# Kernel tuning notes

Hardware: AMD Instinct MI355X
Metric: run time of the kernel (lower is better)

Reference implementation:

```python
import jax, jax.numpy as jnp
import numpy as np

B, T, S, D = 8, 16, 256, 1024
H, KVH, HD = 16, 4, 64
GROUPS = H // KVH
SCALE = HD ** -0.5
CAP = 50.0
EPS = 1e-6


def setup_inputs() -> dict:
    key = jax.random.key(0)
    ks = jax.random.split(key, 5)
    return {
        "x": jax.random.normal(ks[0], (B, T, S, D), dtype=jnp.float32),
        "Wq": jax.random.normal(ks[1], (D, H * HD), dtype=jnp.float32) * (D ** -0.5),
        "Wk": jax.random.normal(ks[2], (D, KVH * HD), dtype=jnp.float32) * (D ** -0.5),
        "Wv": jax.random.normal(ks[3], (D, KVH * HD), dtype=jnp.float32) * (D ** -0.5),
        "Wo": jax.random.normal(ks[4], (H * HD, D), dtype=jnp.float32) * ((H * HD) ** -0.5),
        "q_norm_w": jnp.ones((HD,), dtype=jnp.float32),
        "k_norm_w": jnp.ones((HD,), dtype=jnp.float32),
    }


def _rmsnorm(x, w):
    rms = jnp.sqrt(jnp.mean(x * x, axis=-1, keepdims=True) + EPS)
    return x / rms * w


def reference(x, Wq, Wk, Wv, Wo, q_norm_w, k_norm_w):
    b, t, s, d = x.shape
    xf = x.reshape(b * t, s, d)                    # (BT, S, D)
    q = (xf @ Wq).reshape(b * t, s, H, HD).transpose(0, 2, 1, 3)   # (BT, H, S, hd)
    k = (xf @ Wk).reshape(b * t, s, KVH, HD).transpose(0, 2, 1, 3)  # (BT, KVH, S, hd)
    v = (xf @ Wv).reshape(b * t, s, KVH, HD).transpose(0, 2, 1, 3)
    q = _rmsnorm(q, q_norm_w)
    k = _rmsnorm(k, k_norm_w)
    if GROUPS > 1:
        k = jnp.repeat(k, GROUPS, axis=1)          # (BT, H, S, hd)
        v = jnp.repeat(v, GROUPS, axis=1)
    logits = jnp.einsum("bhqd,bhkd->bhqk", q, k) * SCALE
    logits = CAP * jnp.tanh(logits / CAP)          # soft cap
    attn = jax.nn.softmax(logits, axis=-1)
    out = jnp.einsum("bhqk,bhkd->bhqd", attn, v)   # (BT, H, S, hd)
    out = out.transpose(0, 2, 1, 3).reshape(b * t, s, H * HD)
    out = out @ Wo
    return out.reshape(b, t, s, d)
```

## Files before the change

### kernel.cpp

```cpp
#include <hip/hip_runtime.h>
#include <cstdint>
#include <cstddef>

typedef __bf16 bf16x8 __attribute__((ext_vector_type(8)));
typedef float f32x4 __attribute__((ext_vector_type(4)));
typedef unsigned short u16;
typedef unsigned short u16x8 __attribute__((ext_vector_type(8)));

#define ROWS 32768
#define DMODEL 1024
#define NQKV 1536
#define SCALE_ 0.125f
#define CAP_ 50.0f

__device__ __forceinline__ u16 f2bf(float f) {
    unsigned u = __float_as_uint(f);
    u += 0x7fffu + ((u >> 16) & 1u);
    return (u16)(u >> 16);
}
__device__ __forceinline__ float bf2f(u16 b) {
    return __uint_as_float(((unsigned)b) << 16);
}

__global__ __launch_bounds__(256) void f32_to_bf16_vec(
    const float* __restrict__ in, u16* __restrict__ out, int n4)
{
    int i = blockIdx.x * 256 + threadIdx.x;
    if (i >= n4) return;
    float4 f = ((const float4*)in)[i];
    ushort4 u;
    u.x = f2bf(f.x); u.y = f2bf(f.y); u.z = f2bf(f.z); u.w = f2bf(f.w);
    ((ushort4*)out)[i] = u;
}

__global__ __launch_bounds__(256) void transpose_bf16(
    const float* __restrict__ src, u16* __restrict__ dst, int R, int C)
{
    __shared__ float tile[32][33];
    int c0 = blockIdx.x * 32;
    int r0 = blockIdx.y * 32;
    int tx = threadIdx.x & 31;
    int ty = threadIdx.x >> 5;
#pragma unroll
    for (int i = 0; i < 32; i += 8)
        tile[ty + i][tx] = src[(size_t)(r0 + ty + i) * C + (c0 + tx)];
    __syncthreads();
#pragma unroll
    for (int i = 0; i < 32; i += 8)
        dst[(size_t)(c0 + ty + i) * R + (r0 + tx)] = f2bf(tile[tx][ty + i]);
}

template<bool BF16OUT>
__global__ __launch_bounds__(256) void gemm_bt(
    const u16* __restrict__ A, const u16* __restrict__ Bt,
    void* __restrict__ Cout, int M, int N, int K)
{
    __shared__ u16 As[128][32];
    __shared__ u16 Bs[128][32];
    const int tid  = threadIdx.x;
    const int wave = tid >> 6;
    const int lane = tid & 63;
    const int q4   = lane >> 4;
    const int cl   = lane & 15;
    const int wr   = wave >> 1, wc = wave & 1;
    const int m0   = blockIdx.x * 128;
    const int n0   = blockIdx.y * 128;
    const int srow = lane >> 2;
    const int skoff = (lane & 3) * 8;

    const f32x4 zero = {0.f, 0.f, 0.f, 0.f};
    f32x4 acc[4][4];
#pragma unroll
    for (int i = 0; i < 4; ++i)
#pragma unroll
        for (int j = 0; j < 4; ++j) acc[i][j] = zero;

    for (int k0 = 0; k0 < K; k0 += 32) {
        __syncthreads();
#pragma unroll
        for (int cc = 0; cc < 2; ++cc) {
            int r = 32 * wave + 16 * cc + srow;
            const u16* ga = A + (size_t)(m0 + r) * K + k0 + skoff;
            __builtin_amdgcn_global_load_lds(
                (const __attribute__((address_space(1))) void*)ga,
                (__attribute__((address_space(3))) void*)(&As[32 * wave + 16 * cc][0]),
                16, 0, 0);
            const u16* gb = Bt + (size_t)(n0 + r) * K + k0 + skoff;
            __builtin_amdgcn_global_load_lds(
                (const __attribute__((address_space(1))) void*)gb,
                (__attribute__((address_space(3))) void*)(&Bs[32 * wave + 16 * cc][0]),
                16, 0, 0);
        }
        __syncthreads();
        bf16x8 af[4], bfr[4];
#pragma unroll
        for (int i = 0; i < 4; ++i)
            af[i] = *(const bf16x8*)&As[64 * wr + 16 * i + cl][q4 * 8];
#pragma unroll
        for (int j = 0; j < 4; ++j)
            bfr[j] = *(const bf16x8*)&Bs[64 * wc + 16 * j + cl][q4 * 8];
#pragma unroll
        for (int i = 0; i < 4; ++i)
#pragma unroll
            for (int j = 0; j < 4; ++j)
                acc[i][j] = __builtin_amdgcn_mfma_f32_16x16x32_bf16(
                    af[i], bfr[j], acc[i][j], 0, 0, 0);
    }

#pragma unroll
    for (int i = 0; i < 4; ++i)
#pragma unroll
        for (int j = 0; j < 4; ++j)
#pragma unroll
            for (int r = 0; r < 4; ++r) {
                int row = m0 + 64 * wr + 16 * i + q4 * 4 + r;
                int col = n0 + 64 * wc + 16 * j + cl;
                if (BF16OUT)
                    ((u16*)Cout)[(size_t)row * N + col] = f2bf(acc[i][j][r]);
                else
                    ((float*)Cout)[(size_t)row * N + col] = acc[i][j][r];
            }
}

__global__ __launch_bounds__(256) void rmsnorm_qk(
    u16* __restrict__ qkv, const float* __restrict__ qw, const float* __restrict__ kw)
{
    int gid = blockIdx.x * 16 + (threadIdx.x >> 4);
    int l16 = threadIdx.x & 15;
    int row = gid / 20;
    int hc  = gid - row * 20;
    const float* w = (hc < 16) ? qw : kw;
    size_t base = (size_t)row * NQKV + hc * 64;
    u16* p = qkv + base + l16 * 4;
    uint2 d = *(const uint2*)p;
    float f0 = bf2f((u16)(d.x & 0xffff));
    float f1 = bf2f((u16)(d.x >> 16));
    float f2 = bf2f((u16)(d.y & 0xffff));
    float f3 = bf2f((u16)(d.y >> 16));
    float ss = f0 * f0 + f1 * f1 + f2 * f2 + f3 * f3;
#pragma unroll
    for (int off = 1; off < 16; off <<= 1) ss += __shfl_xor(ss, off, 64);
    float r = rsqrtf(ss * (1.0f / 64.0f) + 1e-6f);
    float w0 = w[l16 * 4 + 0], w1 = w[l16 * 4 + 1];
    float w2 = w[l16 * 4 + 2], w3 = w[l16 * 4 + 3];
    uint2 o;
    o.x = (unsigned)f2bf(f0 * r * w0) | ((unsigned)f2bf(f1 * r * w1) << 16);
    o.y = (unsigned)f2bf(f2 * r * w2) | ((unsigned)f2bf(f3 * r * w3) << 16);
    *(uint2*)p = o;
}

__global__ __launch_bounds__(256, 2) void attention_kernel(
    const u16* __restrict__ qkv, u16* __restrict__ ao)
{
    const int bi  = blockIdx.x;
    const int bt  = bi >> 4;
    const int h   = bi & 15;
    const int kvh = h >> 2;
    const int tid  = threadIdx.x;
    const int wave = tid >> 6;
    const int lane = tid & 63;
    const int q4   = lane >> 4;
    const int cl   = lane & 15;

    __shared__ u16 Vt[64][264];
    __shared__ u16 P[4][64][72];

    {
        const u16* vrow = qkv + (size_t)(bt * 256 + tid) * NQKV + 1280 + kvh * 64;
#pragma unroll
        for (int ch = 0; ch < 8; ++ch) {
            u16x8 v8 = *(const u16x8*)(vrow + ch * 8);
#pragma unroll
            for (int e = 0; e < 8; ++e) Vt[ch * 8 + e][tid] = v8[e];
        }
    }
    __syncthreads();

    const u16* qbase = qkv + (size_t)(bt * 256) * NQKV + h * 64;
    const u16* kbase = qkv + (size_t)(bt * 256) * NQKV + 1024 + kvh * 64;

    const f32x4 zero = {0.f, 0.f, 0.f, 0.f};
    f32x4 o[4][4];
    float m_[4][4], l_[4][4];
#pragma unroll
    for (int i = 0; i < 4; ++i)
#pragma unroll
        for (int r = 0; r < 4; ++r) { m_[i][r] = -1e30f; l_[i][r] = 0.f; }
#pragma unroll
    for (int i = 0; i < 4; ++i)
#pragma unroll
        for (int j = 0; j < 4; ++j) o[i][j] = zero;

    for (int nb = 0; nb < 4; ++nb) {
        f32x4 s[4][4];
#pragma unroll
        for (int i = 0; i < 4; ++i)
#pragma unroll
            for (int j = 0; j < 4; ++j) s[i][j] = zero;

#pragma unroll
        for (int ks = 0; ks < 2; ++ks) {
            bf16x8 qa[4], kb[4];
#pragma unroll
            for (int i = 0; i < 4; ++i)
                qa[i] = *(const bf16x8*)(qbase +
                    (size_t)(wave * 64 + 16 * i + cl) * NQKV + ks * 32 + q4 * 8);
#pragma unroll
            for (int j = 0; j < 4; ++j)
                kb[j] = *(const bf16x8*)(kbase +
                    (size_t)(nb * 64 + 16 * j + cl) * NQKV + ks * 32 + q4 * 8);
#pragma unroll
            for (int i = 0; i < 4; ++i)
#pragma unroll
                for (int j = 0; j < 4; ++j)
                    s[i][j] = __builtin_amdgcn_mfma_f32_16x16x32_bf16(
                        qa[i], kb[j], s[i][j], 0, 0, 0);
        }

        float bm[4][4];
#pragma unroll
        for (int i = 0; i < 4; ++i)
#pragma unroll
            for (int r = 0; r < 4; ++r) bm[i][r] = -1e30f;
#pragma unroll
        for (int i = 0; i < 4; ++i)
#pragma unroll
            for (int j = 0; j < 4; ++j)
#pragma unroll
                for (int r = 0; r < 4; ++r) {
                    float y = s[i][j][r] * (SCALE_ / CAP_);
                    float e = __expf(2.0f * y);
                    float capped = CAP_ * (1.0f - 2.0f / (e + 1.0f));
                    s[i][j][r] = capped;
                    bm[i][r] = fmaxf(bm[i][r], capped);
                }
#pragma unroll
        for (int off = 1; off < 16; off <<= 1)
#pragma unroll
            for (int i = 0; i < 4; ++i)
#pragma unroll
                for (int r = 0; r < 4; ++r)
                    bm[i][r] = fmaxf(bm[i][r], __shfl_xor(bm[i][r], off, 64));

        float alpha[4][4];
#pragma unroll
        for (int i = 0; i < 4; ++i)
#pragma unroll
            for (int r = 0; r < 4; ++r) {
                float mn = fmaxf(m_[i][r], bm[i][r]);
                alpha[i][r] = __expf(m_[i][r] - mn);
                m_[i][r] = mn;
            }
#pragma unroll
        for (int i = 0; i < 4; ++i)
#pragma unroll
            for (int j = 0; j < 4; ++j)
#pragma unroll
                for (int r = 0; r < 4; ++r) o[i][j][r] *= alpha[i][r];

        float rs[4][4];
#pragma unroll
        for (int i = 0; i < 4; ++i)
#pragma unroll
            for (int r = 0; r < 4; ++r) rs[i][r] = 0.f;
#pragma unroll
        for (int i = 0; i < 4; ++i)
#pragma unroll
            for (int j = 0; j < 4; ++j)
#pragma unroll
                for (int r = 0; r < 4; ++r) {
                    float p = __expf(s[i][j][r] - m_[i][r]);
                    s[i][j][r] = p;
                    rs[i][r] += p;
                }
#pragma unroll
        for (int off = 1; off < 16; off <<= 1)
#pragma unroll
            for (int i = 0; i < 4; ++i)
#pragma unroll
                for (int r = 0; r < 4; ++r) rs[i][r] += __shfl_xor(rs[i][r], off, 64);
#pragma unroll
        for (int i = 0; i < 4; ++i)
#pragma unroll
            for (int r = 0; r < 4; ++r) l_[i][r] = l_[i][r] * alpha[i][r] + rs[i][r];

#pragma unroll
        for (int i = 0; i < 4; ++i)
#pragma unroll
            for (int j = 0; j < 4; ++j)
#pragma unroll
                for (int r = 0; r < 4; ++r)
                    P[wave][16 * i + q4 * 4 + r][16 * j + cl] = f2bf(s[i][j][r]);
        __syncthreads();

#pragma unroll
        for (int ks = 0; ks < 2; ++ks) {
            bf16x8 pa[4], vb[4];
#pragma unroll
            for (int i = 0; i < 4; ++i)
                pa[i] = *(const bf16x8*)&P[wave][16 * i + cl][ks * 32 + q4 * 8];
#pragma unroll
            for (int j = 0; j < 4; ++j)
                vb[j] = *(const bf16x8*)&Vt[16 * j + cl][nb * 64 + ks * 32 + q4 * 8];
#pragma unroll
            for (int i = 0; i < 4; ++i)
#pragma unroll
                for (int j = 0; j < 4; ++j)
                    o[i][j] = __builtin_amdgcn_mfma_f32_16x16x32_bf16(
                        pa[i], vb[j], o[i][j], 0, 0, 0);
        }
    }

#pragma unroll
    for (int i = 0; i < 4; ++i)
#pragma unroll
        for (int r = 0; r < 4; ++r) {
            float inv = 1.0f / l_[i][r];
            int row = bt * 256 + wave * 64 + 16 * i + q4 * 4 + r;
#pragma unroll
            for (int j = 0; j < 4; ++j) {
                int col = h * 64 + 16 * j + cl;
                ao[(size_t)row * DMODEL + col] = f2bf(o[i][j][r] * inv);
            }
        }
}

extern "C" void kernel_launch(void* const* d_in, const int* in_sizes, int n_in,
                              void* d_out, int out_size, void* d_ws, size_t ws_size,
                              hipStream_t stream)
{
    const float* x  = (const float*)d_in[0];
    const float* Wq = (const float*)d_in[1];
    const float* Wk = (const float*)d_in[2];
    const float* Wv = (const float*)d_in[3];
    const float* Wo = (const float*)d_in[4];
    const float* qw = (const float*)d_in[5];
    const float* kw = (const float*)d_in[6];
    float* out = (float*)d_out;

    char* ws = (char*)d_ws;
    u16* Xb  = (u16*)(ws);
    u16* QKV = (u16*)(ws + (size_t)67108864);
    u16* AO  = (u16*)(ws + (size_t)167772160);
    u16* WcT = (u16*)(ws + (size_t)234881024);
    u16* WoT = (u16*)(ws + (size_t)238026752);

    f32_to_bf16_vec<<<dim3(32768), dim3(256), 0, stream>>>(x, Xb, 8388608);
    transpose_bf16<<<dim3(32, 32), dim3(256), 0, stream>>>(Wq, WcT, 1024, 1024);
    transpose_bf16<<<dim3(8, 32), dim3(256), 0, stream>>>(Wk, WcT + (size_t)1024 * 1024, 1024, 256);
    transpose_bf16<<<dim3(8, 32), dim3(256), 0, stream>>>(Wv, WcT + (size_t)1280 * 1024, 1024, 256);
    transpose_bf16<<<dim3(32, 32), dim3(256), 0, stream>>>(Wo, WoT, 1024, 1024);
    gemm_bt<true><<<dim3(256, 12), dim3(256), 0, stream>>>(Xb, WcT, (void*)QKV, ROWS, NQKV, 1024);
    rmsnorm_qk<<<dim3(40960), dim3(256), 0, stream>>>(QKV, qw, kw);
    attention_kernel<<<dim3(2048), dim3(256), 0, stream>>>(QKV, AO);
    gemm_bt<false><<<dim3(256, 8), dim3(256), 0, stream>>>(AO, WoT, (void*)out, ROWS, DMODEL, 1024);
}
```

Measured before the change: 683.3 us.

## Fuse QK RMSNorm into attention and use a fixed-max softcap softmax

Removes the separate rmsnorm_qk pass. Per-row Q and K RMS scales are now computed inside the attention kernel and applied to the logits, with the norm weights folded into Q. Because tanh soft-capping bounds the logits, online max tracking and rescaling are replaced by exponentiating the capped logit directly with exp2/rcp intrinsics. Row sums are computed with an MFMA against a ones vector instead of shuffles. The P tile shrinks, the block-wide barrier is dropped, and occupancy is raised to 3 blocks per SIMD; the risks are exp values up to e^50 being held in bf16 and extra register pressure.

```diff
diff --git a/kernel.cpp b/kernel.cpp
--- a/kernel.cpp
+++ b/kernel.cpp
@@ -5,21 +5,25 @@
 typedef __bf16 bf16x8 __attribute__((ext_vector_type(8)));
 typedef float f32x4 __attribute__((ext_vector_type(4)));
 typedef unsigned short u16;
+typedef unsigned int u32;
 typedef unsigned short u16x8 __attribute__((ext_vector_type(8)));
 
 #define ROWS 32768
 #define DMODEL 1024
 #define NQKV 1536
-#define SCALE_ 0.125f
-#define CAP_ 50.0f
+#define C1_ 0.0072134752044448170f
+#define A2_ 144.26950408889634f
+#define B2_ 72.13475204444817f
 
 __device__ __forceinline__ u16 f2bf(float f) {
     unsigned u = __float_as_uint(f);
     u += 0x7fffu + ((u >> 16) & 1u);
     return (u16)(u >> 16);
 }
-__device__ __forceinline__ float bf2f(u16 b) {
-    return __uint_as_float(((unsigned)b) << 16);
+__device__ __forceinline__ float bf_lo(u32 u) { return __uint_as_float(u << 16); }
+__device__ __forceinline__ float bf_hi(u32 u) { return __uint_as_float(u & 0xffff0000u); }
+__device__ __forceinline__ u32 pack_rne(float lo, float hi) {
+    return (u32)f2bf(lo) | ((u32)f2bf(hi) << 16);
 }
 
 __global__ __launch_bounds__(256) void f32_to_bf16_vec(
@@ -122,35 +126,9 @@
             }
 }
 
-__global__ __launch_bounds__(256) void rmsnorm_qk(
-    u16* __restrict__ qkv, const float* __restrict__ qw, const float* __restrict__ kw)
-{
-    int gid = blockIdx.x * 16 + (threadIdx.x >> 4);
-    int l16 = threadIdx.x & 15;
-    int row = gid / 20;
-    int hc  = gid - row * 20;
-    const float* w = (hc < 16) ? qw : kw;
-    size_t base = (size_t)row * NQKV + hc * 64;
-    u16* p = qkv + base + l16 * 4;
-    uint2 d = *(const uint2*)p;
-    float f0 = bf2f((u16)(d.x & 0xffff));
-    float f1 = bf2f((u16)(d.x >> 16));
-    float f2 = bf2f((u16)(d.y & 0xffff));
-    float f3 = bf2f((u16)(d.y >> 16));
-    float ss = f0 * f0 + f1 * f1 + f2 * f2 + f3 * f3;
-#pragma unroll
-    for (int off = 1; off < 16; off <<= 1) ss += __shfl_xor(ss, off, 64);
-    float r = rsqrtf(ss * (1.0f / 64.0f) + 1e-6f);
-    float w0 = w[l16 * 4 + 0], w1 = w[l16 * 4 + 1];
-    float w2 = w[l16 * 4 + 2], w3 = w[l16 * 4 + 3];
-    uint2 o;
-    o.x = (unsigned)f2bf(f0 * r * w0) | ((unsigned)f2bf(f1 * r * w1) << 16);
-    o.y = (unsigned)f2bf(f2 * r * w2) | ((unsigned)f2bf(f3 * r * w3) << 16);
-    *(uint2*)p = o;
-}
-
-__global__ __launch_bounds__(256, 2) void attention_kernel(
-    const u16* __restrict__ qkv, u16* __restrict__ ao)
+__global__ __launch_bounds__(256, 3) void attention_kernel(
+    const u16* __restrict__ qkv, const float* __restrict__ qw,
+    const float* __restrict__ kw, u16* __restrict__ ao)
 {
     const int bi  = blockIdx.x;
     const int bt  = bi >> 4;
@@ -162,8 +140,8 @@
     const int q4   = lane >> 4;
     const int cl   = lane & 15;
 
-    __shared__ u16 Vt[64][264];
-    __shared__ u16 P[4][64][72];
+    __shared__ __align__(16) u16 Vt[64][264];
+    __shared__ __align__(16) u16 P[4][64][40];
 
     {
         const u16* vrow = qkv + (size_t)(bt * 256 + tid) * NQKV + 1280 + kvh * 64;
@@ -179,143 +157,128 @@
     const u16* qbase = qkv + (size_t)(bt * 256) * NQKV + h * 64;
     const u16* kbase = qkv + (size_t)(bt * 256) * NQKV + 1024 + kvh * 64;
 
+    uint4 qa[2][4];
+    float rq[4];
+    float wqk[2][8];
+#pragma unroll
+    for (int ks = 0; ks < 2; ++ks)
+#pragma unroll
+        for (int e = 0; e < 8; ++e) {
+            int d = ks * 32 + q4 * 8 + e;
+            wqk[ks][e] = qw[d] * kw[d];
+        }
+#pragma unroll
+    for (int i = 0; i < 4; ++i) {
+#pragma unroll
+        for (int ks = 0; ks < 2; ++ks)
+            qa[ks][i] = *(const uint4*)(qbase +
+                (size_t)(wave * 64 + 16 * i + cl) * NQKV + ks * 32 + q4 * 8);
+        float ss = 0.f;
+#pragma unroll
+        for (int ks = 0; ks < 2; ++ks) {
+            const u32* u = (const u32*)&qa[ks][i];
+#pragma unroll
+            for (int e = 0; e < 4; ++e) {
+                float lo = bf_lo(u[e]), hi = bf_hi(u[e]);
+                ss += lo * lo + hi * hi;
+            }
+        }
+        ss += __shfl_xor(ss, 16, 64);
+        ss += __shfl_xor(ss, 32, 64);
+        rq[i] = rsqrtf(ss * (1.0f / 64.0f) + 1e-6f);
+#pragma unroll
+        for (int ks = 0; ks < 2; ++ks) {
+            u32* u = (u32*)&qa[ks][i];
+#pragma unroll
+            for (int e = 0; e < 4; ++e) {
+                float lo = bf_lo(u[e]) * wqk[ks][2 * e];
+                float hi = bf_hi(u[e]) * wqk[ks][2 * e + 1];
+                u[e] = pack_rne(lo, hi);
+            }
+        }
+    }
+    float rqc[4][4];
+#pragma unroll
+    for (int i = 0; i < 4; ++i)
+#pragma unroll
+        for (int r = 0; r < 4; ++r)
+            rqc[i][r] = __shfl(rq[i], 4 * q4 + r, 64);
+
     const f32x4 zero = {0.f, 0.f, 0.f, 0.f};
     f32x4 o[4][4];
-    float m_[4][4], l_[4][4];
+    f32x4 lacc[4];
+#pragma unroll
+    for (int i = 0; i < 4; ++i) {
+        lacc[i] = zero;
+#pragma unroll
+        for (int j = 0; j < 4; ++j) o[i][j] = zero;
+    }
+    bf16x8 ones;
+#pragma unroll
+    for (int e = 0; e < 8; ++e) ones[e] = (__bf16)1.0f;
+
+    for (int nb = 0; nb < 4; ++nb) {
+#pragma unroll
+        for (int jh = 0; jh < 2; ++jh) {
+#pragma unroll
+            for (int jj = 0; jj < 2; ++jj) {
+                const int j = 2 * jh + jj;
+                uint4 kb[2];
+#pragma unroll
+                for (int ks = 0; ks < 2; ++ks)
+                    kb[ks] = *(const uint4*)(kbase +
+                        (size_t)(nb * 64 + 16 * j + cl) * NQKV + ks * 32 + q4 * 8);
+                float ss = 0.f;
+#pragma unroll
+                for (int ks = 0; ks < 2; ++ks) {
+                    const u32* u = (const u32*)&kb[ks];
+#pragma unroll
+                    for (int e = 0; e < 4; ++e) {
+                        float lo = bf_lo(u[e]), hi = bf_hi(u[e]);
+                        ss += lo * lo + hi * hi;
+                    }
+                }
+                ss += __shfl_xor(ss, 16, 64);
+                ss += __shfl_xor(ss, 32, 64);
+                float rkc1 = rsqrtf(ss * (1.0f / 64.0f) + 1e-6f) * C1_;
+
+#pragma unroll
+                for (int i = 0; i < 4; ++i) {
+                    f32x4 s = __builtin_amdgcn_mfma_f32_16x16x32_bf16(
+                        *(const bf16x8*)&qa[0][i], *(const bf16x8*)&kb[0], zero, 0, 0, 0);
+                    s = __builtin_amdgcn_mfma_f32_16x16x32_bf16(
+                        *(const bf16x8*)&qa[1][i], *(const bf16x8*)&kb[1], s, 0, 0, 0);
+#pragma unroll
+                    for (int r = 0; r < 4; ++r) {
+                        float e2 = __builtin_amdgcn_exp2f(s[r] * rqc[i][r] * rkc1);
+                        float rc = __builtin_amdgcn_rcpf(e2 + 1.0f);
+                        float p  = __builtin_amdgcn_exp2f(fmaf(-A2_, rc, B2_));
+                        P[wave][16 * i + q4 * 4 + r][16 * jj + cl] = f2bf(p);
+                    }
+                }
+            }
+            bf16x8 vb[4];
+#pragma unroll
+            for (int j2 = 0; j2 < 4; ++j2)
+                vb[j2] = *(const bf16x8*)&Vt[16 * j2 + cl][nb * 64 + jh * 32 + q4 * 8];
+#pragma unroll
+            for (int i = 0; i < 4; ++i) {
+                bf16x8 pa = *(const bf16x8*)&P[wave][16 * i + cl][q4 * 8];
+#pragma unroll
+                for (int j2 = 0; j2 < 4; ++j2)
+                    o[i][j2] = __builtin_amdgcn_mfma_f32_16x16x32_bf16(
+                        pa, vb[j2], o[i][j2], 0, 0, 0);
+                lacc[i] = __builtin_amdgcn_mfma_f32_16x16x32_bf16(
+                    pa, ones, lacc[i], 0, 0, 0);
+            }
+        }
+    }
+
 #pragma unroll
     for (int i = 0; i < 4; ++i)
 #pragma unroll
-        for (int r = 0; r < 4; ++r) { m_[i][r] = -1e30f; l_[i][r] = 0.f; }
-#pragma unroll
-    for (int i = 0; i < 4; ++i)
-#pragma unroll
-        for (int j = 0; j < 4; ++j) o[i][j] = zero;
-
-    for (int nb = 0; nb < 4; ++nb) {
-        f32x4 s[4][4];
-#pragma unroll
-        for (int i = 0; i < 4; ++i)
-#pragma unroll
-            for (int j = 0; j < 4; ++j) s[i][j] = zero;
-
-#pragma unroll
-        for (int ks = 0; ks < 2; ++ks) {
-            bf16x8 qa[4], kb[4];
-#pragma unroll
-            for (int i = 0; i < 4; ++i)
-                qa[i] = *(const bf16x8*)(qbase +
-                    (size_t)(wave * 64 + 16 * i + cl) * NQKV + ks * 32 + q4 * 8);
-#pragma unroll
-            for (int j = 0; j < 4; ++j)
-                kb[j] = *(const bf16x8*)(kbase +
-                    (size_t)(nb * 64 + 16 * j + cl) * NQKV + ks * 32 + q4 * 8);
-#pragma unroll
-            for (int i = 0; i < 4; ++i)
-#pragma unroll
-                for (int j = 0; j < 4; ++j)
-                    s[i][j] = __builtin_amdgcn_mfma_f32_16x16x32_bf16(
-                        qa[i], kb[j], s[i][j], 0, 0, 0);
-        }
-
-        float bm[4][4];
-#pragma unroll
-        for (int i = 0; i < 4; ++i)
-#pragma unroll
-            for (int r = 0; r < 4; ++r) bm[i][r] = -1e30f;
-#pragma unroll
-        for (int i = 0; i < 4; ++i)
-#pragma unroll
-            for (int j = 0; j < 4; ++j)
-#pragma unroll
-                for (int r = 0; r < 4; ++r) {
-                    float y = s[i][j][r] * (SCALE_ / CAP_);
-                    float e = __expf(2.0f * y);
-                    float capped = CAP_ * (1.0f - 2.0f / (e + 1.0f));
-                    s[i][j][r] = capped;
-                    bm[i][r] = fmaxf(bm[i][r], capped);
-                }
-#pragma unroll
-        for (int off = 1; off < 16; off <<= 1)
-#pragma unroll
-            for (int i = 0; i < 4; ++i)
-#pragma unroll
-                for (int r = 0; r < 4; ++r)
-                    bm[i][r] = fmaxf(bm[i][r], __shfl_xor(bm[i][r], off, 64));
-
-        float alpha[4][4];
-#pragma unroll
-        for (int i = 0; i < 4; ++i)
-#pragma unroll
-            for (int r = 0; r < 4; ++r) {
-                float mn = fmaxf(m_[i][r], bm[i][r]);
-                alpha[i][r] = __expf(m_[i][r] - mn);
-                m_[i][r] = mn;
-            }
-#pragma unroll
-        for (int i = 0; i < 4; ++i)
-#pragma unroll
-            for (int j = 0; j < 4; ++j)
-#pragma unroll
-                for (int r = 0; r < 4; ++r) o[i][j][r] *= alpha[i][r];
-
-        float rs[4][4];
-#pragma unroll
-        for (int i = 0; i < 4; ++i)
-#pragma unroll
-            for (int r = 0; r < 4; ++r) rs[i][r] = 0.f;
-#pragma unroll
-        for (int i = 0; i < 4; ++i)
-#pragma unroll
-            for (int j = 0; j < 4; ++j)
-#pragma unroll
-                for (int r = 0; r < 4; ++r) {
-                    float p = __expf(s[i][j][r] - m_[i][r]);
-                    s[i][j][r] = p;
-                    rs[i][r] += p;
-                }
-#pragma unroll
-        for (int off = 1; off < 16; off <<= 1)
-#pragma unroll
-            for (int i = 0; i < 4; ++i)
-#pragma unroll
-                for (int r = 0; r < 4; ++r) rs[i][r] += __shfl_xor(rs[i][r], off, 64);
-#pragma unroll
-        for (int i = 0; i < 4; ++i)
-#pragma unroll
-            for (int r = 0; r < 4; ++r) l_[i][r] = l_[i][r] * alpha[i][r] + rs[i][r];
-
-#pragma unroll
-        for (int i = 0; i < 4; ++i)
-#pragma unroll
-            for (int j = 0; j < 4; ++j)
-#pragma unroll
-                for (int r = 0; r < 4; ++r)
-                    P[wave][16 * i + q4 * 4 + r][16 * j + cl] = f2bf(s[i][j][r]);
-        __syncthreads();
-
-#pragma unroll
-        for (int ks = 0; ks < 2; ++ks) {
-            bf16x8 pa[4], vb[4];
-#pragma unroll
-            for (int i = 0; i < 4; ++i)
-                pa[i] = *(const bf16x8*)&P[wave][16 * i + cl][ks * 32 + q4 * 8];
-#pragma unroll
-            for (int j = 0; j < 4; ++j)
-                vb[j] = *(const bf16x8*)&Vt[16 * j + cl][nb * 64 + ks * 32 + q4 * 8];
-#pragma unroll
-            for (int i = 0; i < 4; ++i)
-#pragma unroll
-                for (int j = 0; j < 4; ++j)
-                    o[i][j] = __builtin_amdgcn_mfma_f32_16x16x32_bf16(
-                        pa[i], vb[j], o[i][j], 0, 0, 0);
-        }
-    }
-
-#pragma unroll
-    for (int i = 0; i < 4; ++i)
-#pragma unroll
         for (int r = 0; r < 4; ++r) {
-            float inv = 1.0f / l_[i][r];
+            float inv = 1.0f / lacc[i][r];
             int row = bt * 256 + wave * 64 + 16 * i + q4 * 4 + r;
 #pragma unroll
             for (int j = 0; j < 4; ++j) {
@@ -351,7 +314,6 @@
     transpose_bf16<<<dim3(8, 32), dim3(256), 0, stream>>>(Wv, WcT + (size_t)1280 * 1024, 1024, 256);
     transpose_bf16<<<dim3(32, 32), dim3(256), 0, stream>>>(Wo, WoT, 1024, 1024);
     gemm_bt<true><<<dim3(256, 12), dim3(256), 0, stream>>>(Xb, WcT, (void*)QKV, ROWS, NQKV, 1024);
-    rmsnorm_qk<<<dim3(40960), dim3(256), 0, stream>>>(QKV, qw, kw);
-    attention_kernel<<<dim3(2048), dim3(256), 0, stream>>>(QKV, AO);
+    attention_kernel<<<dim3(2048), dim3(256), 0, stream>>>(QKV, qw, kw, AO);
     gemm_bt<false><<<dim3(256, 8), dim3(256), 0, stream>>>(AO, WoT, (void*)out, ROWS, DMODEL, 1024);
 }
```

After: 660.1 us. -3.4%, faster.
